# Kernel tuning notes

Hardware: AMD Instinct MI355X
Metric: run time of the kernel (lower is better)

The kernel has to match this reference:

```python
import jax, jax.numpy as jnp
from jax import lax
import numpy as np

W_SSIM = 0.5
W_SMOOTH = 0.1
W_LR = 1.0
C1 = 0.01 ** 2
C2 = 0.03 ** 2


def avg3(x):
    # 3x3 stride-1 VALID average pool (matches F.avg_pool2d(x, 3, 1))
    return lax.reduce_window(x, 0.0, lax.add, (1, 1, 3, 3), (1, 1, 1, 1), 'VALID') / 9.0


def resize_ac(img, oh, ow):
    # bilinear resize with align_corners=True, separable gathers
    B, C, H, W = img.shape
    ys = jnp.linspace(0.0, H - 1.0, oh)
    xs = jnp.linspace(0.0, W - 1.0, ow)
    y0 = jnp.floor(ys).astype(jnp.int32); y1 = jnp.minimum(y0 + 1, H - 1); wy = ys - y0
    x0 = jnp.floor(xs).astype(jnp.int32); x1 = jnp.minimum(x0 + 1, W - 1); wx = xs - x0
    r = img[:, :, y0, :] * (1.0 - wy)[None, None, :, None] + img[:, :, y1, :] * wy[None, None, :, None]
    return r[:, :, :, x0] * (1.0 - wx) + r[:, :, :, x1] * wx


def warp_h(img, disp, sign):
    # horizontal bilinear warp: sample img at x + sign*disp (disp in units of image width),
    # align_corners=True pixel mapping, zeros padding outside the image.
    B, C, H, W = img.shape
    xb = jnp.linspace(0.0, 1.0, W)
    px = (xb[None, None, :] + sign * disp[:, 0, :, :]) * (W - 1)  # [B,H,W] pixel coords
    x0 = jnp.floor(px); f = px - x0
    x0i = x0.astype(jnp.int32); x1i = x0i + 1
    v0 = ((x0i >= 0) & (x0i < W)).astype(img.dtype)
    v1 = ((x1i >= 0) & (x1i < W)).astype(img.dtype)
    i0 = jnp.broadcast_to(jnp.clip(x0i, 0, W - 1)[:, None], (B, C, H, W))
    i1 = jnp.broadcast_to(jnp.clip(x1i, 0, W - 1)[:, None], (B, C, H, W))
    g0 = jnp.take_along_axis(img, i0, axis=3)
    g1 = jnp.take_along_axis(img, i1, axis=3)
    return g0 * (v0 * (1.0 - f))[:, None] + g1 * (v1 * f)[:, None]


def ssim(x, y):
    mu_x = avg3(x); mu_y = avg3(y)
    sig_x = avg3(x * x) - mu_x ** 2
    sig_y = avg3(y * y) - mu_y ** 2
    sig_xy = avg3(x * y) - mu_x * mu_y
    s = ((2 * mu_x * mu_y + C1) * (2 * sig_xy + C2)) / ((mu_x ** 2 + mu_y ** 2 + C1) * (sig_x + sig_y + C2))
    return jnp.clip((1.0 - s) / 2.0, 0.0, 1.0)


def smoothness(disp, img):
    dgx = disp[:, :, :, :-1] - disp[:, :, :, 1:]
    dgy = disp[:, :, :-1, :] - disp[:, :, 1:, :]
    igx = img[:, :, :, :-1] - img[:, :, :, 1:]
    igy = img[:, :, :-1, :] - img[:, :, 1:, :]
    wx = jnp.exp(-jnp.mean(jnp.abs(igx), axis=1, keepdims=True))
    wy = jnp.exp(-jnp.mean(jnp.abs(igy), axis=1, keepdims=True))
    return jnp.mean(jnp.abs(dgx * wx)) + jnp.mean(jnp.abs(dgy * wy))


def compute_loss(disps, left, right):
    B, _, H, W = left.shape
    img_loss = 0.0
    lr_loss = 0.0
    sm_loss = 0.0
    for i, d in enumerate(disps):
        r = 2 ** i
        h, w = H // r, W // r
        lpy = left if i == 0 else resize_ac(left, h, w)
        rpy = right if i == 0 else resize_ac(right, h, w)
        dl = d[:, 0:1]; dr = d[:, 1:2]
        left_est = warp_h(rpy, dl, -1.0)
        right_est = warp_h(lpy, dr, 1.0)
        rl_disp = warp_h(dr, dl, -1.0)
        lr_disp = warp_h(dl, dr, 1.0)
        l1_l = jnp.mean(jnp.abs(left_est - lpy))
        l1_r = jnp.mean(jnp.abs(right_est - rpy))
        ss_l = jnp.mean(ssim(left_est, lpy))
        ss_r = jnp.mean(ssim(right_est, rpy))
        img_loss = img_loss + W_SSIM * ss_l + (1 - W_SSIM) * l1_l + W_SSIM * ss_r + (1 - W_SSIM) * l1_r
        lr_loss = lr_loss + jnp.mean(jnp.abs(rl_disp - dl)) + jnp.mean(jnp.abs(lr_disp - dr))
        sm_loss = sm_loss + (smoothness(dl, lpy) + smoothness(dr, rpy)) / r
    return img_loss + W_SMOOTH * sm_loss + W_LR * lr_loss


def setup_inputs() -> dict:
    key = jax.random.key(0)
    ks = jax.random.split(key, 6)
    B, H, W = 16, 384, 768
    inp = {}
    for i in range(4):
        r = 2 ** i
        # disparities in units of image width; scaled to realistic ~[0, 0.1]
        inp[f'disp{i}'] = jax.random.uniform(ks[i], (B, 2, H // r, W // r), dtype=jnp.float32) * 0.1
    inp['left_image'] = jax.random.uniform(ks[4], (B, 3, H, W), dtype=jnp.float32)
    inp['right_image'] = jax.random.uniform(ks[5], (B, 3, H, W), dtype=jnp.float32)
    return inp


def reference(disp0, disp1, disp2, disp3, left_image, right_image):
    return compute_loss([disp0, disp1, disp2, disp3], left_image, right_image)
```

## Files before the change

### kernel.cpp

```cpp
#include <hip/hip_runtime.h>
#include <math.h>

#define C1F 1.0e-4f
#define C2F 9.0e-4f
#define TX 64
#define TY 4
#define NROWS (TY + 2)
#define NSTAGE ((TY + 2) * (TX + 2))
#define LPAD 4


struct ScaleArgs {
    const float* disp;
    const float* lp;
    const float* rp;
    int h, w, nx, ny, blk0, accoff, ntiles;
    float dmax;
};

__device__ __forceinline__ float2 f2(float v) { return make_float2(v, v); }

__device__ __forceinline__ void warp_coeffs(float px, int W, int& i0, int& i1,
                                            float& w0, float& w1) {
    float x0f = floorf(px);
    float f = px - x0f;
    int x0i = (int)x0f;
    int x1i = x0i + 1;
    float v0 = (x0i >= 0 && x0i < W) ? 1.f : 0.f;
    float v1 = (x1i >= 0 && x1i < W) ? 1.f : 0.f;
    i0 = min(max(x0i, 0), W - 1);
    i1 = min(max(x1i, 0), W - 1);
    w0 = v0 * (1.f - f);
    w1 = v1 * f;
}

template<int N>
__device__ __forceinline__ void block_acc(const float* vals, float* gacc) {
    __shared__ float sacc[N];
    if (threadIdx.x < N) sacc[threadIdx.x] = 0.f;
    __syncthreads();
#pragma unroll
    for (int k = 0; k < N; ++k) {
        float v = vals[k];
#pragma unroll
        for (int off = 32; off > 0; off >>= 1) v += __shfl_down(v, off, 64);
        if ((threadIdx.x & 63) == 0) atomicAdd(&sacc[k], v);
    }
    __syncthreads();
    if (threadIdx.x < N) atomicAdd(&gacc[threadIdx.x], sacc[threadIdx.x]);
}

__device__ __forceinline__ int xcd_swz(int orig, int n) {
    int q = n >> 3, r = n & 7;
    int x = orig & 7;
    int base = (x < r) ? x * (q + 1) : r * (q + 1) + (x - r) * q;
    return base + (orig >> 3);
}

__global__ void k_zero(float* acc) {
    if (threadIdx.x < 64) acc[threadIdx.x] = 0.f;
}

__device__ __forceinline__ bool rng_ok(float v, float dmax) {
    return (v >= 0.f) && (v <= dmax);
}

template<int SW, int RPAD>
__device__ void fused_tile(const ScaleArgs& sa, int t, float* __restrict__ accbase,
                           float* __restrict__ sL, float* __restrict__ sR,
                           float* __restrict__ sdl, float* __restrict__ sdr,
                           float2* __restrict__ simg, int* __restrict__ sok) {
    constexpr int SW4 = SW / 4;
    const int h = sa.h, w = sa.w;
    float* acc = accbase + sa.accoff;

    const int tileX = t % sa.nx;
    int t2 = t / sa.nx;
    const int tileY = t2 % sa.ny;
    const int b = t2 / sa.ny;

    const int xo0 = tileX * TX, yo0 = tileY * TY;
    const int tid = threadIdx.x;
    const float Wm1 = (float)(w - 1);
    const float invWm1 = 1.f / Wm1;
    const int chs = h * w;
    const int lx0 = xo0 - LPAD;
    const int rx0 = xo0 - RPAD;
    const int gy0 = yo0 - 1;
    const float dmax = sa.dmax;

    const float* __restrict__ dl_base = sa.disp + (b * 2 + 0) * chs;
    const float* __restrict__ dr_base = sa.disp + (b * 2 + 1) * chs;
    const float* __restrict__ limg = sa.lp + b * 3 * chs;
    const float* __restrict__ rimg = sa.rp + b * 3 * chs;

    if (tid == 0) *sok = 1;
    __syncthreads();

    bool bad = false;
    const bool xint = (rx0 >= 0) && (lx0 + SW <= w);
    if (xint) {
        for (int i = tid; i < NROWS * SW4; i += 256) {
            int r = i / SW4, k4 = i - r * SW4;
            int y = min(max(gy0 + r, 0), h - 1);
            int goL = y * w + lx0 + 4 * k4;
            int goR = y * w + rx0 + 4 * k4;
            int so = r * SW + 4 * k4;
#pragma unroll
            for (int c = 0; c < 3; ++c) {
                *(float4*)(sL + c * (NROWS * SW) + so) =
                    *(const float4*)(limg + c * chs + goL);
                *(float4*)(sR + c * (NROWS * SW) + so) =
                    *(const float4*)(rimg + c * chs + goR);
            }
            float4 vdl = *(const float4*)(dl_base + goL);
            float4 vdr = *(const float4*)(dr_base + goR);
            *(float4*)(sdl + so) = vdl;
            *(float4*)(sdr + so) = vdr;
            bad = bad || !rng_ok(vdl.x, dmax) || !rng_ok(vdl.y, dmax) ||
                         !rng_ok(vdl.z, dmax) || !rng_ok(vdl.w, dmax) ||
                         !rng_ok(vdr.x, dmax) || !rng_ok(vdr.y, dmax) ||
                         !rng_ok(vdr.z, dmax) || !rng_ok(vdr.w, dmax);
        }
    } else {
        for (int i = tid; i < NROWS * SW; i += 256) {
            int r = i / SW, k = i - r * SW;
            int y = min(max(gy0 + r, 0), h - 1);
            int xl = min(max(lx0 + k, 0), w - 1);
            int xr = min(max(rx0 + k, 0), w - 1);
            int yw = y * w;
#pragma unroll
            for (int c = 0; c < 3; ++c) {
                sL[c * (NROWS * SW) + i] = limg[c * chs + yw + xl];
                sR[c * (NROWS * SW) + i] = rimg[c * chs + yw + xr];
            }
            float vdl = dl_base[yw + xl];
            float vdr = dr_base[yw + xr];
            sdl[i] = vdl;
            sdr[i] = vdr;
            bad = bad || !rng_ok(vdl, dmax) || !rng_ok(vdr, dmax);
        }
    }
    if (bad) *sok = 0;
    __syncthreads();
    const bool ok = (*sok != 0);

    for (int i = tid; i < NSTAGE; i += 256) {
        int sx = i % (TX + 2);
        int sy = i / (TX + 2);
        int x = min(max(xo0 - 1 + sx, 0), w - 1);
        float dl = sdl[sy * SW + (x - lx0)];
        float dr = sdr[sy * SW + (x - rx0)];
        float xb = (float)x * invWm1;
        int i0L, i1L, i0R, i1R;
        float w0L, w1L, w0R, w1R;
        warp_coeffs((xb - dl) * Wm1, w, i0L, i1L, w0L, w1L);
        warp_coeffs((xb + dr) * Wm1, w, i0R, i1R, w0R, w1R);
        if (ok) {
            int a0 = i0L - rx0, a1 = i1L - rx0;
            int b0 = i0R - lx0, b1 = i1R - lx0;
#pragma unroll
            for (int c = 0; c < 3; ++c) {
                const float* R = sR + (c * NROWS + sy) * SW;
                const float* L = sL + (c * NROWS + sy) * SW;
                simg[c * NSTAGE + i] =
                    make_float2(R[a0] * w0L + R[a1] * w1L,
                                L[b0] * w0R + L[b1] * w1R);
            }
        } else {
            int y = min(max(gy0 + sy, 0), h - 1);
            int rowoff = y * w;
#pragma unroll
            for (int c = 0; c < 3; ++c) {
                int co = c * chs + rowoff;
                simg[c * NSTAGE + i] =
                    make_float2(rimg[co + i0L] * w0L + rimg[co + i1L] * w1L,
                                limg[co + i0R] * w0R + limg[co + i1R] * w1R);
            }
        }
    }
    __syncthreads();

    float sums[8] = {0.f, 0.f, 0.f, 0.f, 0.f, 0.f, 0.f, 0.f};
    const int tx = tid & (TX - 1), ty = tid >> 6;
    const int x = xo0 + tx, y = yo0 + ty;
    if (x < w && y < h) {
        const int s = (ty + 1) * (TX + 2) + tx + 1;
        const int rowd = (ty + 1) * SW;
        const int kL = tx + LPAD;
        const int kR = tx + RPAD;
        float dl = sdl[rowd + kL];
        float dr = sdr[rowd + kR];
#pragma unroll
        for (int c = 0; c < 3; ++c) {
            float2 e = simg[c * NSTAGE + s];
            float lv = sL[(c * NROWS + ty + 1) * SW + kL];
            float rv = sR[(c * NROWS + ty + 1) * SW + kR];
            sums[0] += fabsf(e.x - lv);
            sums[1] += fabsf(e.y - rv);
        }
        {
            float xb = (float)x * invWm1;
            int i0, i1; float w0, w1;
            warp_coeffs((xb - dl) * Wm1, w, i0, i1, w0, w1);
            float rl;
            if (ok) {
                rl = sdr[rowd + (i0 - rx0)] * w0 + sdr[rowd + (i1 - rx0)] * w1;
            } else {
                const float* drr = dr_base + y * w;
                rl = drr[i0] * w0 + drr[i1] * w1;
            }
            sums[2] += fabsf(rl - dl);
            warp_coeffs((xb + dr) * Wm1, w, i0, i1, w0, w1);
            float lr;
            if (ok) {
                lr = sdl[rowd + (i0 - lx0)] * w0 + sdl[rowd + (i1 - lx0)] * w1;
            } else {
                const float* dlr = dl_base + y * w;
                lr = dlr[i0] * w0 + dlr[i1] * w1;
            }
            sums[3] += fabsf(lr - dr);
        }
        const float third = 1.f / 3.f;
        if (x < w - 1) {
            float dlx = sdl[rowd + kL + 1], drx = sdr[rowd + kR + 1];
            float ax = 0.f, ay = 0.f;
#pragma unroll
            for (int c = 0; c < 3; ++c) {
                const float* Lr = sL + (c * NROWS + ty + 1) * SW;
                const float* Rr = sR + (c * NROWS + ty + 1) * SW;
                ax += fabsf(Lr[kL] - Lr[kL + 1]);
                ay += fabsf(Rr[kR] - Rr[kR + 1]);
            }
            sums[4] += fabsf(dl - dlx) * __expf(-ax * third) +
                       fabsf(dr - drx) * __expf(-ay * third);
        }
        if (y < h - 1) {
            float dly = sdl[rowd + SW + kL], dry = sdr[rowd + SW + kR];
            float ax = 0.f, ay = 0.f;
#pragma unroll
            for (int c = 0; c < 3; ++c) {
                const float* Lr0 = sL + (c * NROWS + ty + 1) * SW;
                const float* Lr1 = Lr0 + SW;
                const float* Rr0 = sR + (c * NROWS + ty + 1) * SW;
                const float* Rr1 = Rr0 + SW;
                ax += fabsf(Lr0[kL] - Lr1[kL]);
                ay += fabsf(Rr0[kR] - Rr1[kR]);
            }
            sums[5] += fabsf(dl - dly) * __expf(-ax * third) +
                       fabsf(dr - dry) * __expf(-ay * third);
        }
        if (x >= 1 && x <= w - 2 && y >= 1 && y <= h - 2) {
            const float2 inv9 = f2(1.f / 9.f);
            const float2 c1 = f2(C1F), c2 = f2(C2F);
            const float2 two = f2(2.f), one = f2(1.f), half_ = f2(0.5f);
#pragma unroll 1
            for (int c = 0; c < 3; ++c) {
                float2 sX = f2(0.f), sY = f2(0.f);
                float2 sXX = f2(0.f), sYY = f2(0.f), sXY = f2(0.f);
#pragma unroll
                for (int dy = 0; dy < 3; ++dy) {
                    const float2* eS = simg + c * NSTAGE + (ty + dy) * (TX + 2);
                    const float* Lr = sL + (c * NROWS + ty + dy) * SW;
                    const float* Rr = sR + (c * NROWS + ty + dy) * SW;
#pragma unroll
                    for (int dx = 0; dx < 3; ++dx) {
                        float2 a = eS[tx + dx];
                        float lv = Lr[tx + dx + LPAD - 1];
                        float rv = Rr[tx + dx + RPAD - 1];
                        sX.x += a.x;  sX.y += a.y;
                        sY.x += lv;   sY.y += rv;
                        sXX.x += a.x * a.x;  sXX.y += a.y * a.y;
                        sYY.x += lv * lv;    sYY.y += rv * rv;
                        sXY.x += a.x * lv;   sXY.y += a.y * rv;
                    }
                }
                float2 mx = make_float2(sX.x * inv9.x, sX.y * inv9.y);
                float2 my = make_float2(sY.x * inv9.x, sY.y * inv9.y);
                float2 vx = make_float2(sXX.x * inv9.x - mx.x * mx.x,
                                        sXX.y * inv9.y - mx.y * mx.y);
                float2 vy = make_float2(sYY.x * inv9.x - my.x * my.x,
                                        sYY.y * inv9.y - my.y * my.y);
                float2 vxy = make_float2(sXY.x * inv9.x - mx.x * my.x,
                                         sXY.y * inv9.y - mx.y * my.y);
                float2 num = make_float2((two.x * mx.x * my.x + c1.x) * (two.x * vxy.x + c2.x),
                                         (two.y * mx.y * my.y + c1.y) * (two.y * vxy.y + c2.y));
                float2 den = make_float2((mx.x * mx.x + my.x * my.x + c1.x) * (vx.x + vy.x + c2.x),
                                         (mx.y * mx.y + my.y * my.y + c1.y) * (vx.y + vy.y + c2.y));
                float2 ss = make_float2(num.x * __builtin_amdgcn_rcpf(den.x),
                                        num.y * __builtin_amdgcn_rcpf(den.y));
                float2 v = make_float2((one.x - ss.x) * half_.x,
                                       (one.y - ss.y) * half_.y);
                sums[6] += fminf(fmaxf(v.x, 0.f), 1.f);
                sums[7] += fminf(fmaxf(v.y, 0.f), 1.f);
            }
        }
    }
    block_acc<8>(sums, acc);
}

#define SW0 152
#define RP0 84
#define SWB 112
#define RPB 44

__global__ void __launch_bounds__(256, 4)
k_fused0_resize(ScaleArgs s0, float* __restrict__ accbase,
                const float* __restrict__ left, const float* __restrict__ right,
                float* __restrict__ lo1, float* __restrict__ ro1,
                float* __restrict__ lo2, float* __restrict__ ro2,
                float* __restrict__ lo3, float* __restrict__ ro3,
                int B, int H, int W,
                int nFusedBlocks, long long n1, long long n2, long long n3) {
    __shared__ __align__(16) float sL[3 * NROWS * SW0];
    __shared__ __align__(16) float sR[3 * NROWS * SW0];
    __shared__ __align__(16) float sdl[NROWS * SW0];
    __shared__ __align__(16) float sdr[NROWS * SW0];
    __shared__ __align__(16) float2 simg[3 * NSTAGE];
    __shared__ int sok;

    if ((int)blockIdx.x < nFusedBlocks) {
        int t = xcd_swz((int)blockIdx.x, nFusedBlocks);
        fused_tile<SW0, RP0>(s0, t, accbase, sL, sR, sdl, sdr, simg, &sok);
        return;
    }
    long long idx = (long long)(blockIdx.x - nFusedBlocks) * blockDim.x + threadIdx.x;
    int oh, ow;
    float* lo;
    float* ro;
    if (idx < n1) {
        oh = H / 2; ow = W / 2; lo = lo1; ro = ro1;
    } else if (idx < n1 + n2) {
        idx -= n1; oh = H / 4; ow = W / 4; lo = lo2; ro = ro2;
    } else if (idx < n1 + n2 + n3) {
        idx -= n1 + n2; oh = H / 8; ow = W / 8; lo = lo3; ro = ro3;
    } else {
        return;
    }
    long long half = (long long)B * 3 * oh * ow;
    const float* src = left;
    float* dst = lo;
    if (idx >= half) { src = right; dst = ro; idx -= half; }
    int x = (int)(idx % ow);
    long long t = idx / ow;
    int y = (int)(t % oh);
    t /= oh;
    int c = (int)(t % 3);
    int b = (int)(t / 3);
    float sy = (float)(H - 1) / (float)(oh - 1);
    float sx = (float)(W - 1) / (float)(ow - 1);
    float fy = y * sy;
    float fx = x * sx;
    int y0 = (int)floorf(fy); float wy = fy - (float)y0;
    int x0 = (int)floorf(fx); float wx = fx - (float)x0;
    int y1 = min(y0 + 1, H - 1); y0 = min(y0, H - 1);
    int x1 = min(x0 + 1, W - 1); x0 = min(x0, W - 1);
    const float* p = src + ((long long)b * 3 + c) * H * W;
    float a00 = p[(long long)y0 * W + x0];
    float a10 = p[(long long)y1 * W + x0];
    float a01 = p[(long long)y0 * W + x1];
    float a11 = p[(long long)y1 * W + x1];
    float r0 = a00 * (1.f - wy) + a10 * wy;
    float r1 = a01 * (1.f - wy) + a11 * wy;
    dst[(((long long)b * 3 + c) * oh + y) * ow + x] = r0 * (1.f - wx) + r1 * wx;
}

__global__ void __launch_bounds__(256, 5)
k_fused_small(ScaleArgs s1, ScaleArgs s2, ScaleArgs s3,
              float* __restrict__ accbase) {
    __shared__ __align__(16) float sL[3 * NROWS * SWB];
    __shared__ __align__(16) float sR[3 * NROWS * SWB];
    __shared__ __align__(16) float sdl[NROWS * SWB];
    __shared__ __align__(16) float sdr[NROWS * SWB];
    __shared__ __align__(16) float2 simg[3 * NSTAGE];
    __shared__ int sok;

    ScaleArgs sa;
    {
        int blk = (int)blockIdx.x;
        if (blk >= s3.blk0)      sa = s3;
        else if (blk >= s2.blk0) sa = s2;
        else                     sa = s1;
    }
    int t = xcd_swz((int)blockIdx.x - sa.blk0, sa.ntiles);
    fused_tile<SWB, RPB>(sa, t, accbase, sL, sR, sdl, sdr, simg, &sok);
}

__global__ void k_final(const float* __restrict__ acc, float* __restrict__ out,
                        int B, int H, int W) {
    if (threadIdx.x != 0 || blockIdx.x != 0) return;
    float img = 0.f, lr = 0.f, sm = 0.f;
    for (int i = 0; i < 4; ++i) {
        int r = 1 << i;
        int h = H / r, w = W / r;
        const float* a = acc + i * 8;
        float Nl1 = (float)B * 3.f * (float)h * (float)w;
        float Nss = (float)B * 3.f * (float)(h - 2) * (float)(w - 2);
        float Nlr = (float)B * (float)h * (float)w;
        float Nsx = (float)B * (float)h * (float)(w - 1);
        float Nsy = (float)B * (float)(h - 1) * (float)w;
        img += 0.5f * (a[6] / Nss) + 0.5f * (a[0] / Nl1)
             + 0.5f * (a[7] / Nss) + 0.5f * (a[1] / Nl1);
        lr += a[2] / Nlr + a[3] / Nlr;
        sm += (a[4] / Nsx + a[5] / Nsy) / (float)r;
    }
    out[0] = img + 0.1f * sm + 1.0f * lr;
}

extern "C" void kernel_launch(void* const* d_in, const int* in_sizes, int n_in,
                              void* d_out, int out_size, void* d_ws, size_t ws_size,
                              hipStream_t stream) {
    const int B = 16, H = 384, W = 768;
    const float* disp[4] = {(const float*)d_in[0], (const float*)d_in[1],
                            (const float*)d_in[2], (const float*)d_in[3]};
    const float* left = (const float*)d_in[4];
    const float* right = (const float*)d_in[5];
    float* out = (float*)d_out;

    float* acc = (float*)d_ws;
    float* pyr = acc + 256;
    long long sz1 = (long long)B * 3 * (H / 2) * (W / 2);
    long long sz2 = (long long)B * 3 * (H / 4) * (W / 4);
    long long sz3 = (long long)B * 3 * (H / 8) * (W / 8);
    float* lp1 = pyr;
    float* rp1 = lp1 + sz1;
    float* lp2 = rp1 + sz1;
    float* rp2 = lp2 + sz2;
    float* lp3 = rp2 + sz2;
    float* rp3 = lp3 + sz3;

    const int TB = 256;
    const float* lp[4] = {left, lp1, lp2, lp3};
    const float* rp[4] = {right, rp1, rp2, rp3};
    const float reach_tab[4] = {78.f, 40.f, 40.f, 40.f};
    ScaleArgs sa[4];
    for (int i = 0; i < 4; ++i) {
        int r = 1 << i;
        int h = H / r, w = W / r;
        sa[i].disp = disp[i];
        sa[i].lp = lp[i];
        sa[i].rp = rp[i];
        sa[i].h = h;
        sa[i].w = w;
        sa[i].nx = (w + TX - 1) / TX;
        sa[i].ny = (h + TY - 1) / TY;
        sa[i].accoff = i * 8;
        sa[i].ntiles = sa[i].nx * sa[i].ny * B;
        sa[i].blk0 = 0;
        sa[i].dmax = reach_tab[i] / (float)(w - 1);
    }

    hipLaunchKernelGGL(k_zero, dim3(1), dim3(64), 0, stream, acc);

    {
        int nFused = sa[0].ntiles;
        long long n1 = 2 * sz1, n2 = 2 * sz2, n3 = 2 * sz3;
        long long nrElem = n1 + n2 + n3;
        int nResize = (int)((nrElem + TB - 1) / TB);
        hipLaunchKernelGGL(k_fused0_resize, dim3((unsigned)(nFused + nResize)), dim3(TB), 0, stream,
                           sa[0], acc, left, right, lp1, rp1, lp2, rp2, lp3, rp3,
                           B, H, W, nFused, n1, n2, n3);
    }

    {
        int b1 = sa[1].ntiles;
        int b2 = sa[2].ntiles;
        int b3 = sa[3].ntiles;
        sa[1].blk0 = 0;
        sa[2].blk0 = b1;
        sa[3].blk0 = b1 + b2;
        hipLaunchKernelGGL(k_fused_small, dim3((unsigned)(b1 + b2 + b3)), dim3(TB), 0, stream,
                           sa[1], sa[2], sa[3], acc);
    }
    hipLaunchKernelGGL(k_final, dim3(1), dim3(64), 0, stream, acc, out, B, H, W);
}
```

Before: 518.1 us.

## Pack warped and source pixels into float4 staging and hardcode resize shapes

The shared staging buffer now holds float4 entries that pair each warped pixel with its source pixels, so the SSIM window and the smoothness gradients read one vector load instead of several scattered scalar reads. Interior tiles use an unclamped warp-coefficient path when the disparity range check passes. The resize blocks are moved ahead of the fused tiles and use compile-time shapes to avoid runtime division. Launch bounds are lowered to 3 blocks because the float4 staging doubles that buffer's shared memory. The cost is higher LDS use and lower occupancy, and the resize is now hardcoded to B=16 at 384x768.

```diff
diff --git a/kernel.cpp b/kernel.cpp
--- a/kernel.cpp
+++ b/kernel.cpp
@@ -34,6 +34,16 @@
     w1 = v1 * f;
 }
 
+__device__ __forceinline__ void warp_coeffs_safe(float px, int& i0, int& i1,
+                                                 float& w0, float& w1) {
+    float x0f = floorf(px);
+    float f = px - x0f;
+    i0 = (int)x0f;
+    i1 = i0 + 1;
+    w0 = 1.f - f;
+    w1 = f;
+}
+
 template<int N>
 __device__ __forceinline__ void block_acc(const float* vals, float* gacc) {
     __shared__ float sacc[N];
@@ -65,11 +75,11 @@
     return (v >= 0.f) && (v <= dmax);
 }
 
-template<int SW, int RPAD>
+template<int SW, int RPAD, int REACH>
 __device__ void fused_tile(const ScaleArgs& sa, int t, float* __restrict__ accbase,
                            float* __restrict__ sL, float* __restrict__ sR,
                            float* __restrict__ sdl, float* __restrict__ sdr,
-                           float2* __restrict__ simg, int* __restrict__ sok) {
+                           float4* __restrict__ simg, int* __restrict__ sok) {
     constexpr int SW4 = SW / 4;
     const int h = sa.h, w = sa.w;
     float* acc = accbase + sa.accoff;
@@ -144,28 +154,38 @@
     if (bad) *sok = 0;
     __syncthreads();
     const bool ok = (*sok != 0);
+    const bool use_safe = ok && xint && (xo0 >= REACH + 1) &&
+                          (xo0 + TX + REACH + 1 <= w);
 
     for (int i = tid; i < NSTAGE; i += 256) {
         int sx = i % (TX + 2);
         int sy = i / (TX + 2);
-        int x = min(max(xo0 - 1 + sx, 0), w - 1);
+        int xr_ = xo0 - 1 + sx;
+        int x = use_safe ? xr_ : min(max(xr_, 0), w - 1);
         float dl = sdl[sy * SW + (x - lx0)];
         float dr = sdr[sy * SW + (x - rx0)];
         float xb = (float)x * invWm1;
         int i0L, i1L, i0R, i1R;
         float w0L, w1L, w0R, w1R;
-        warp_coeffs((xb - dl) * Wm1, w, i0L, i1L, w0L, w1L);
-        warp_coeffs((xb + dr) * Wm1, w, i0R, i1R, w0R, w1R);
+        if (use_safe) {
+            warp_coeffs_safe((xb - dl) * Wm1, i0L, i1L, w0L, w1L);
+            warp_coeffs_safe((xb + dr) * Wm1, i0R, i1R, w0R, w1R);
+        } else {
+            warp_coeffs((xb - dl) * Wm1, w, i0L, i1L, w0L, w1L);
+            warp_coeffs((xb + dr) * Wm1, w, i0R, i1R, w0R, w1R);
+        }
         if (ok) {
             int a0 = i0L - rx0, a1 = i1L - rx0;
             int b0 = i0R - lx0, b1 = i1R - lx0;
+            int xl = x - lx0, xr2 = x - rx0;
 #pragma unroll
             for (int c = 0; c < 3; ++c) {
                 const float* R = sR + (c * NROWS + sy) * SW;
                 const float* L = sL + (c * NROWS + sy) * SW;
                 simg[c * NSTAGE + i] =
-                    make_float2(R[a0] * w0L + R[a1] * w1L,
-                                L[b0] * w0R + L[b1] * w1R);
+                    make_float4(R[a0] * w0L + R[a1] * w1L,
+                                L[b0] * w0R + L[b1] * w1R,
+                                L[xl], R[xr2]);
             }
         } else {
             int y = min(max(gy0 + sy, 0), h - 1);
@@ -174,8 +194,9 @@
             for (int c = 0; c < 3; ++c) {
                 int co = c * chs + rowoff;
                 simg[c * NSTAGE + i] =
-                    make_float2(rimg[co + i0L] * w0L + rimg[co + i1L] * w1L,
-                                limg[co + i0R] * w0R + limg[co + i1R] * w1R);
+                    make_float4(rimg[co + i0L] * w0L + rimg[co + i1L] * w1L,
+                                limg[co + i0R] * w0R + limg[co + i1R] * w1R,
+                                limg[co + x], rimg[co + x]);
             }
         }
     }
@@ -191,18 +212,19 @@
         const int kR = tx + RPAD;
         float dl = sdl[rowd + kL];
         float dr = sdr[rowd + kR];
+        float4 ctr[3];
 #pragma unroll
         for (int c = 0; c < 3; ++c) {
-            float2 e = simg[c * NSTAGE + s];
-            float lv = sL[(c * NROWS + ty + 1) * SW + kL];
-            float rv = sR[(c * NROWS + ty + 1) * SW + kR];
-            sums[0] += fabsf(e.x - lv);
-            sums[1] += fabsf(e.y - rv);
+            float4 v = simg[c * NSTAGE + s];
+            ctr[c] = v;
+            sums[0] += fabsf(v.x - v.z);
+            sums[1] += fabsf(v.y - v.w);
         }
         {
             float xb = (float)x * invWm1;
             int i0, i1; float w0, w1;
-            warp_coeffs((xb - dl) * Wm1, w, i0, i1, w0, w1);
+            if (use_safe) warp_coeffs_safe((xb - dl) * Wm1, i0, i1, w0, w1);
+            else          warp_coeffs((xb - dl) * Wm1, w, i0, i1, w0, w1);
             float rl;
             if (ok) {
                 rl = sdr[rowd + (i0 - rx0)] * w0 + sdr[rowd + (i1 - rx0)] * w1;
@@ -211,7 +233,8 @@
                 rl = drr[i0] * w0 + drr[i1] * w1;
             }
             sums[2] += fabsf(rl - dl);
-            warp_coeffs((xb + dr) * Wm1, w, i0, i1, w0, w1);
+            if (use_safe) warp_coeffs_safe((xb + dr) * Wm1, i0, i1, w0, w1);
+            else          warp_coeffs((xb + dr) * Wm1, w, i0, i1, w0, w1);
             float lr;
             if (ok) {
                 lr = sdl[rowd + (i0 - lx0)] * w0 + sdl[rowd + (i1 - lx0)] * w1;
@@ -227,10 +250,9 @@
             float ax = 0.f, ay = 0.f;
 #pragma unroll
             for (int c = 0; c < 3; ++c) {
-                const float* Lr = sL + (c * NROWS + ty + 1) * SW;
-                const float* Rr = sR + (c * NROWS + ty + 1) * SW;
-                ax += fabsf(Lr[kL] - Lr[kL + 1]);
-                ay += fabsf(Rr[kR] - Rr[kR + 1]);
+                float4 v1 = simg[c * NSTAGE + s + 1];
+                ax += fabsf(ctr[c].z - v1.z);
+                ay += fabsf(ctr[c].w - v1.w);
             }
             sums[4] += fabsf(dl - dlx) * __expf(-ax * third) +
                        fabsf(dr - drx) * __expf(-ay * third);
@@ -240,12 +262,9 @@
             float ax = 0.f, ay = 0.f;
 #pragma unroll
             for (int c = 0; c < 3; ++c) {
-                const float* Lr0 = sL + (c * NROWS + ty + 1) * SW;
-                const float* Lr1 = Lr0 + SW;
-                const float* Rr0 = sR + (c * NROWS + ty + 1) * SW;
-                const float* Rr1 = Rr0 + SW;
-                ax += fabsf(Lr0[kL] - Lr1[kL]);
-                ay += fabsf(Rr0[kR] - Rr1[kR]);
+                float4 v1 = simg[c * NSTAGE + s + (TX + 2)];
+                ax += fabsf(ctr[c].z - v1.z);
+                ay += fabsf(ctr[c].w - v1.w);
             }
             sums[5] += fabsf(dl - dly) * __expf(-ax * third) +
                        fabsf(dr - dry) * __expf(-ay * third);
@@ -260,19 +279,15 @@
                 float2 sXX = f2(0.f), sYY = f2(0.f), sXY = f2(0.f);
 #pragma unroll
                 for (int dy = 0; dy < 3; ++dy) {
-                    const float2* eS = simg + c * NSTAGE + (ty + dy) * (TX + 2);
-                    const float* Lr = sL + (c * NROWS + ty + dy) * SW;
-                    const float* Rr = sR + (c * NROWS + ty + dy) * SW;
+                    const float4* eS = simg + c * NSTAGE + (ty + dy) * (TX + 2);
 #pragma unroll
                     for (int dx = 0; dx < 3; ++dx) {
-                        float2 a = eS[tx + dx];
-                        float lv = Lr[tx + dx + LPAD - 1];
-                        float rv = Rr[tx + dx + RPAD - 1];
-                        sX.x += a.x;  sX.y += a.y;
-                        sY.x += lv;   sY.y += rv;
-                        sXX.x += a.x * a.x;  sXX.y += a.y * a.y;
-                        sYY.x += lv * lv;    sYY.y += rv * rv;
-                        sXY.x += a.x * lv;   sXY.y += a.y * rv;
+                        float4 v = eS[tx + dx];
+                        sX.x += v.x;  sX.y += v.y;
+                        sY.x += v.z;  sY.y += v.w;
+                        sXX.x += v.x * v.x;  sXX.y += v.y * v.y;
+                        sYY.x += v.z * v.z;  sYY.y += v.w * v.w;
+                        sXY.x += v.x * v.z;  sXY.y += v.y * v.w;
                     }
                 }
                 float2 mx = make_float2(sX.x * inv9.x, sX.y * inv9.y);
@@ -301,78 +316,87 @@
 
 #define SW0 152
 #define RP0 84
+#define RCH0 78
 #define SWB 112
 #define RPB 44
-
-__global__ void __launch_bounds__(256, 4)
+#define RCHB 40
+
+template<int OH, int OW, int HH, int WW>
+__device__ __forceinline__ void resize_px(long long idx,
+                                          const float* __restrict__ left,
+                                          const float* __restrict__ right,
+                                          float* __restrict__ lo,
+                                          float* __restrict__ ro) {
+    const long long half = (long long)16 * 3 * OH * OW;
+    const float* src = left;
+    float* dst = lo;
+    if (idx >= half) { src = right; dst = ro; idx -= half; }
+    int x = (int)(idx % OW);
+    long long t = idx / OW;
+    int y = (int)(t % OH);
+    t /= OH;
+    int c = (int)(t % 3);
+    int b = (int)(t / 3);
+    constexpr float sy = (float)(HH - 1) / (float)(OH - 1);
+    constexpr float sx = (float)(WW - 1) / (float)(OW - 1);
+    float fy = y * sy;
+    float fx = x * sx;
+    int y0 = (int)floorf(fy); float wy = fy - (float)y0;
+    int x0 = (int)floorf(fx); float wx = fx - (float)x0;
+    int y1 = min(y0 + 1, HH - 1); y0 = min(y0, HH - 1);
+    int x1 = min(x0 + 1, WW - 1); x0 = min(x0, WW - 1);
+    const float* p = src + ((long long)b * 3 + c) * HH * WW;
+    float a00 = p[(long long)y0 * WW + x0];
+    float a10 = p[(long long)y1 * WW + x0];
+    float a01 = p[(long long)y0 * WW + x1];
+    float a11 = p[(long long)y1 * WW + x1];
+    float r0 = a00 * (1.f - wy) + a10 * wy;
+    float r1 = a01 * (1.f - wy) + a11 * wy;
+    dst[(((long long)b * 3 + c) * OH + y) * OW + x] = r0 * (1.f - wx) + r1 * wx;
+}
+
+#define N1E 7077888LL
+#define N2E 1769472LL
+#define N3E 442368LL
+#define NRESB 36288
+
+__global__ void __launch_bounds__(256, 3)
 k_fused0_resize(ScaleArgs s0, float* __restrict__ accbase,
                 const float* __restrict__ left, const float* __restrict__ right,
                 float* __restrict__ lo1, float* __restrict__ ro1,
                 float* __restrict__ lo2, float* __restrict__ ro2,
                 float* __restrict__ lo3, float* __restrict__ ro3,
-                int B, int H, int W,
-                int nFusedBlocks, long long n1, long long n2, long long n3) {
+                int nFusedBlocks) {
     __shared__ __align__(16) float sL[3 * NROWS * SW0];
     __shared__ __align__(16) float sR[3 * NROWS * SW0];
     __shared__ __align__(16) float sdl[NROWS * SW0];
     __shared__ __align__(16) float sdr[NROWS * SW0];
-    __shared__ __align__(16) float2 simg[3 * NSTAGE];
+    __shared__ __align__(16) float4 simg[3 * NSTAGE];
     __shared__ int sok;
 
-    if ((int)blockIdx.x < nFusedBlocks) {
-        int t = xcd_swz((int)blockIdx.x, nFusedBlocks);
-        fused_tile<SW0, RP0>(s0, t, accbase, sL, sR, sdl, sdr, simg, &sok);
+    int blk = (int)blockIdx.x;
+    if (blk < NRESB) {
+        long long idx = (long long)blk * 256 + threadIdx.x;
+        if (idx < N1E)
+            resize_px<192, 384, 384, 768>(idx, left, right, lo1, ro1);
+        else if (idx < N1E + N2E)
+            resize_px<96, 192, 384, 768>(idx - N1E, left, right, lo2, ro2);
+        else
+            resize_px<48, 96, 384, 768>(idx - N1E - N2E, left, right, lo3, ro3);
         return;
     }
-    long long idx = (long long)(blockIdx.x - nFusedBlocks) * blockDim.x + threadIdx.x;
-    int oh, ow;
-    float* lo;
-    float* ro;
-    if (idx < n1) {
-        oh = H / 2; ow = W / 2; lo = lo1; ro = ro1;
-    } else if (idx < n1 + n2) {
-        idx -= n1; oh = H / 4; ow = W / 4; lo = lo2; ro = ro2;
-    } else if (idx < n1 + n2 + n3) {
-        idx -= n1 + n2; oh = H / 8; ow = W / 8; lo = lo3; ro = ro3;
-    } else {
-        return;
-    }
-    long long half = (long long)B * 3 * oh * ow;
-    const float* src = left;
-    float* dst = lo;
-    if (idx >= half) { src = right; dst = ro; idx -= half; }
-    int x = (int)(idx % ow);
-    long long t = idx / ow;
-    int y = (int)(t % oh);
-    t /= oh;
-    int c = (int)(t % 3);
-    int b = (int)(t / 3);
-    float sy = (float)(H - 1) / (float)(oh - 1);
-    float sx = (float)(W - 1) / (float)(ow - 1);
-    float fy = y * sy;
-    float fx = x * sx;
-    int y0 = (int)floorf(fy); float wy = fy - (float)y0;
-    int x0 = (int)floorf(fx); float wx = fx - (float)x0;
-    int y1 = min(y0 + 1, H - 1); y0 = min(y0, H - 1);
-    int x1 = min(x0 + 1, W - 1); x0 = min(x0, W - 1);
-    const float* p = src + ((long long)b * 3 + c) * H * W;
-    float a00 = p[(long long)y0 * W + x0];
-    float a10 = p[(long long)y1 * W + x0];
-    float a01 = p[(long long)y0 * W + x1];
-    float a11 = p[(long long)y1 * W + x1];
-    float r0 = a00 * (1.f - wy) + a10 * wy;
-    float r1 = a01 * (1.f - wy) + a11 * wy;
-    dst[(((long long)b * 3 + c) * oh + y) * ow + x] = r0 * (1.f - wx) + r1 * wx;
-}
-
-__global__ void __launch_bounds__(256, 5)
+    int t = xcd_swz(blk - NRESB, nFusedBlocks);
+    fused_tile<SW0, RP0, RCH0>(s0, t, accbase, sL, sR, sdl, sdr, simg, &sok);
+}
+
+__global__ void __launch_bounds__(256, 3)
 k_fused_small(ScaleArgs s1, ScaleArgs s2, ScaleArgs s3,
               float* __restrict__ accbase) {
     __shared__ __align__(16) float sL[3 * NROWS * SWB];
     __shared__ __align__(16) float sR[3 * NROWS * SWB];
     __shared__ __align__(16) float sdl[NROWS * SWB];
     __shared__ __align__(16) float sdr[NROWS * SWB];
-    __shared__ __align__(16) float2 simg[3 * NSTAGE];
+    __shared__ __align__(16) float4 simg[3 * NSTAGE];
     __shared__ int sok;
 
     ScaleArgs sa;
@@ -383,7 +407,7 @@
         else                     sa = s1;
     }
     int t = xcd_swz((int)blockIdx.x - sa.blk0, sa.ntiles);
-    fused_tile<SWB, RPB>(sa, t, accbase, sL, sR, sdl, sdr, simg, &sok);
+    fused_tile<SWB, RPB, RCHB>(sa, t, accbase, sL, sR, sdl, sdr, simg, &sok);
 }
 
 __global__ void k_final(const float* __restrict__ acc, float* __restrict__ out,
@@ -429,7 +453,6 @@
     float* lp3 = rp2 + sz2;
     float* rp3 = lp3 + sz3;
 
-    const int TB = 256;
     const float* lp[4] = {left, lp1, lp2, lp3};
     const float* rp[4] = {right, rp1, rp2, rp3};
     const float reach_tab[4] = {78.f, 40.f, 40.f, 40.f};
@@ -454,12 +477,9 @@
 
     {
         int nFused = sa[0].ntiles;
-        long long n1 = 2 * sz1, n2 = 2 * sz2, n3 = 2 * sz3;
-        long long nrElem = n1 + n2 + n3;
-        int nResize = (int)((nrElem + TB - 1) / TB);
-        hipLaunchKernelGGL(k_fused0_resize, dim3((unsigned)(nFused + nResize)), dim3(TB), 0, stream,
+        hipLaunchKernelGGL(k_fused0_resize, dim3((unsigned)(NRESB + nFused)), dim3(256), 0, stream,
                            sa[0], acc, left, right, lp1, rp1, lp2, rp2, lp3, rp3,
-                           B, H, W, nFused, n1, n2, n3);
+                           nFused);
     }
 
     {
@@ -469,7 +489,7 @@
         sa[1].blk0 = 0;
         sa[2].blk0 = b1;
         sa[3].blk0 = b1 + b2;
-        hipLaunchKernelGGL(k_fused_small, dim3((unsigned)(b1 + b2 + b3)), dim3(TB), 0, stream,
+        hipLaunchKernelGGL(k_fused_small, dim3((unsigned)(b1 + b2 + b3)), dim3(256), 0, stream,
                            sa[1], sa[2], sa[3], acc);
     }
     hipLaunchKernelGGL(k_final, dim3(1), dim3(64), 0, stream, acc, out, B, H, W);
```

Result: no change. 525.1 us (+1.3%).
